# Performance work log

Measured on AMD Instinct MI355X. Metric: run time of the kernel, lower is better.

The kernel has to match this reference:

```python
import jax, jax.numpy as jnp
import numpy as np

HIDDEN = 2048
EMBED = 512
LEN_ACTION = 64   # total size of the NAS search space (embedding rows)
N_VALUES = 16     # number of choices for the queried parameter's head


def gru_cell(x, h, w_ih, w_hh, b_ih, b_hh):
    # PyTorch GRU cell: gates packed as [r, z, n] along dim 0 of weights
    gi = x @ w_ih.T + b_ih          # [1, 3H]
    gh = h @ w_hh.T + b_hh          # [1, 3H]
    i_r, i_z, i_n = jnp.split(gi, 3, axis=-1)
    h_r, h_z, h_n = jnp.split(gh, 3, axis=-1)
    r = jax.nn.sigmoid(i_r + h_r)
    z = jax.nn.sigmoid(i_z + h_z)
    n = jnp.tanh(i_n + r * h_n)
    return (1.0 - z) * n + z * h


def setup_inputs() -> dict:
    key = jax.random.key(0)
    ks = jax.random.split(key, 14)
    s = 0.02
    return {
        "x": jax.random.randint(ks[0], (1,), 0, LEN_ACTION),
        "h_in": jax.random.normal(ks[1], (2, 1, HIDDEN), jnp.float32),
        "emb": jax.random.normal(ks[2], (LEN_ACTION, EMBED), jnp.float32) * s,
        "w_ih0": jax.random.normal(ks[3], (3 * HIDDEN, EMBED), jnp.float32) * s,
        "w_hh0": jax.random.normal(ks[4], (3 * HIDDEN, HIDDEN), jnp.float32) * s,
        "b_ih0": jax.random.normal(ks[5], (3 * HIDDEN,), jnp.float32) * s,
        "b_hh0": jax.random.normal(ks[6], (3 * HIDDEN,), jnp.float32) * s,
        "w_ih1": jax.random.normal(ks[7], (3 * HIDDEN, HIDDEN), jnp.float32) * s,
        "w_hh1": jax.random.normal(ks[8], (3 * HIDDEN, HIDDEN), jnp.float32) * s,
        "b_ih1": jax.random.normal(ks[9], (3 * HIDDEN,), jnp.float32) * s,
        "b_hh1": jax.random.normal(ks[10], (3 * HIDDEN,), jnp.float32) * s,
        "w_head": jax.random.normal(ks[11], (N_VALUES, HIDDEN), jnp.float32) * s,
        "b_head": jax.random.normal(ks[12], (N_VALUES,), jnp.float32) * s,
    }


def reference(x, h_in, emb, w_ih0, w_hh0, b_ih0, b_hh0,
              w_ih1, w_hh1, b_ih1, b_hh1, w_head, b_head):
    e = emb[x]                                    # [1, E] (seq len 1)
    h0 = gru_cell(e, h_in[0], w_ih0, w_hh0, b_ih0, b_hh0)   # [1, H]
    h1 = gru_cell(h0, h_in[1], w_ih1, w_hh1, b_ih1, b_hh1)  # [1, H]
    logits = h1 @ w_head.T + b_head               # [1, N_VALUES]
    probs = jax.nn.softmax(logits, axis=-1)       # Categorical probs
    h_out = jnp.stack([h0, h1], axis=0)           # [num_layers, 1, H]
    return probs, h_out
```

## Files before the change

kernel.cpp:

```cpp
#include <hip/hip_runtime.h>
#include <math.h>

#define HID 2048
#define EMB 512
#define NV 16

__device__ __forceinline__ float wred(float v) {
#pragma unroll
    for (int o = 32; o >= 1; o >>= 1) v += __shfl_down(v, o, 64);
    return v;
}

__device__ __forceinline__ float dot4(float4 a, float4 b) {
    return a.x * b.x + a.y * b.y + a.z * b.z + a.w * b.w;
}

__device__ __forceinline__ float sig(float x) { return 1.0f / (1.0f + __expf(-x)); }

__global__ __launch_bounds__(256) void k1(
    const int* __restrict__ xidx,
    const float* __restrict__ h_in,
    const float* __restrict__ emb,
    const float* __restrict__ w_ih0,
    const float* __restrict__ w_hh0,
    const float* __restrict__ b_ih0,
    const float* __restrict__ b_hh0,
    const float* __restrict__ w_hh1,
    const float* __restrict__ b_hh1,
    float* __restrict__ out,
    float* __restrict__ gh1)
{
    const int tid  = threadIdx.x;
    const int lane = tid & 63;
    const int wv   = tid >> 6;
    const int bid  = blockIdx.x;
    __shared__ float red[4][6];

    float s0 = 0.f, s1 = 0.f, s2 = 0.f, s3 = 0.f, s4 = 0.f, s5 = 0.f;

    if (bid < HID) {
        const int j = bid;
        const float bi_r = b_ih0[j];
        const float bi_z = b_ih0[j + HID];
        const float bi_n = b_ih0[j + 2 * HID];
        const float bh_r = b_hh0[j];
        const float bh_z = b_hh0[j + HID];
        const float bh_n = b_hh0[j + 2 * HID];
        const float hprev = h_in[j];

        const float4* hv  = (const float4*)h_in;
        const float4* wh0 = (const float4*)(w_hh0 + (size_t)j * HID);
        const float4* wh1 = (const float4*)(w_hh0 + (size_t)(j + HID) * HID);
        const float4* wh2 = (const float4*)(w_hh0 + (size_t)(j + 2 * HID) * HID);

        float4 x0 = hv[tid];
        float4 x1 = hv[tid + 256];
        float4 a0 = wh0[tid];
        float4 a1 = wh0[tid + 256];
        float4 b0 = wh1[tid];
        float4 b1 = wh1[tid + 256];
        float4 d0 = wh2[tid];
        float4 d1 = wh2[tid + 256];

        if (tid < 128) {
            const float4* ev  = (const float4*)(emb + (size_t)xidx[0] * EMB);
            const float4* wi0 = (const float4*)(w_ih0 + (size_t)j * EMB);
            const float4* wi1 = (const float4*)(w_ih0 + (size_t)(j + HID) * EMB);
            const float4* wi2 = (const float4*)(w_ih0 + (size_t)(j + 2 * HID) * EMB);
            float4 e4 = ev[tid];
            float4 ia = wi0[tid];
            float4 ib = wi1[tid];
            float4 ic = wi2[tid];
            s0 = dot4(ia, e4);
            s1 = dot4(ib, e4);
            s2 = dot4(ic, e4);
        }

        s3 = dot4(a0, x0) + dot4(a1, x1);
        s4 = dot4(b0, x0) + dot4(b1, x1);
        s5 = dot4(d0, x0) + dot4(d1, x1);

        s0 = wred(s0); s1 = wred(s1); s2 = wred(s2);
        s3 = wred(s3); s4 = wred(s4); s5 = wred(s5);
        if (lane == 0) {
            red[wv][0] = s0; red[wv][1] = s1; red[wv][2] = s2;
            red[wv][3] = s3; red[wv][4] = s4; red[wv][5] = s5;
        }
        __syncthreads();
        if (tid == 0) {
            float ir  = red[0][0] + red[1][0] + red[2][0] + red[3][0] + bi_r;
            float iz  = red[0][1] + red[1][1] + red[2][1] + red[3][1] + bi_z;
            float inn = red[0][2] + red[1][2] + red[2][2] + red[3][2] + bi_n;
            float hr  = red[0][3] + red[1][3] + red[2][3] + red[3][3] + bh_r;
            float hz  = red[0][4] + red[1][4] + red[2][4] + red[3][4] + bh_z;
            float hn  = red[0][5] + red[1][5] + red[2][5] + red[3][5] + bh_n;
            float r = sig(ir + hr);
            float z = sig(iz + hz);
            float n = tanhf(inn + r * hn);
            out[NV + j] = (1.0f - z) * n + z * hprev;
        }
    } else {
        const int j = bid - HID;
        const float bh_r = b_hh1[j];
        const float bh_z = b_hh1[j + HID];
        const float bh_n = b_hh1[j + 2 * HID];

        const float4* hv  = (const float4*)(h_in + HID);
        const float4* wh0 = (const float4*)(w_hh1 + (size_t)j * HID);
        const float4* wh1 = (const float4*)(w_hh1 + (size_t)(j + HID) * HID);
        const float4* wh2 = (const float4*)(w_hh1 + (size_t)(j + 2 * HID) * HID);

        float4 x0 = hv[tid];
        float4 x1 = hv[tid + 256];
        float4 a0 = wh0[tid];
        float4 a1 = wh0[tid + 256];
        float4 b0 = wh1[tid];
        float4 b1 = wh1[tid + 256];
        float4 d0 = wh2[tid];
        float4 d1 = wh2[tid + 256];

        s0 = dot4(a0, x0) + dot4(a1, x1);
        s1 = dot4(b0, x0) + dot4(b1, x1);
        s2 = dot4(d0, x0) + dot4(d1, x1);

        s0 = wred(s0); s1 = wred(s1); s2 = wred(s2);
        if (lane == 0) {
            red[wv][0] = s0; red[wv][1] = s1; red[wv][2] = s2;
        }
        __syncthreads();
        if (tid == 0) {
            gh1[j]           = red[0][0] + red[1][0] + red[2][0] + red[3][0] + bh_r;
            gh1[j + HID]     = red[0][1] + red[1][1] + red[2][1] + red[3][1] + bh_z;
            gh1[j + 2 * HID] = red[0][2] + red[1][2] + red[2][2] + red[3][2] + bh_n;
        }
    }
}

__global__ __launch_bounds__(256) void k2(
    const float* __restrict__ h_in,
    const float* __restrict__ w_ih1,
    const float* __restrict__ b_ih1,
    const float* __restrict__ gh1,
    float* __restrict__ out)
{
    const int tid  = threadIdx.x;
    const int lane = tid & 63;
    const int wv   = tid >> 6;
    const int j    = blockIdx.x;
    __shared__ float red[4][3];

    const float bi_r = b_ih1[j];
    const float bi_z = b_ih1[j + HID];
    const float bi_n = b_ih1[j + 2 * HID];
    const float g_r  = gh1[j];
    const float g_z  = gh1[j + HID];
    const float g_n  = gh1[j + 2 * HID];
    const float hprev = h_in[HID + j];

    const float4* hv  = (const float4*)(out + NV);
    const float4* wi0 = (const float4*)(w_ih1 + (size_t)j * HID);
    const float4* wi1 = (const float4*)(w_ih1 + (size_t)(j + HID) * HID);
    const float4* wi2 = (const float4*)(w_ih1 + (size_t)(j + 2 * HID) * HID);

    float4 x0 = hv[tid];
    float4 x1 = hv[tid + 256];
    float4 a0 = wi0[tid];
    float4 a1 = wi0[tid + 256];
    float4 b0 = wi1[tid];
    float4 b1 = wi1[tid + 256];
    float4 d0 = wi2[tid];
    float4 d1 = wi2[tid + 256];

    float s0 = dot4(a0, x0) + dot4(a1, x1);
    float s1 = dot4(b0, x0) + dot4(b1, x1);
    float s2 = dot4(d0, x0) + dot4(d1, x1);

    s0 = wred(s0); s1 = wred(s1); s2 = wred(s2);
    if (lane == 0) { red[wv][0] = s0; red[wv][1] = s1; red[wv][2] = s2; }
    __syncthreads();
    if (tid == 0) {
        float ir  = red[0][0] + red[1][0] + red[2][0] + red[3][0] + bi_r;
        float iz  = red[0][1] + red[1][1] + red[2][1] + red[3][1] + bi_z;
        float inn = red[0][2] + red[1][2] + red[2][2] + red[3][2] + bi_n;
        float r = sig(ir + g_r);
        float z = sig(iz + g_z);
        float n = tanhf(inn + r * g_n);
        out[NV + HID + j] = (1.0f - z) * n + z * hprev;
    }
}

__global__ __launch_bounds__(256) void k3(
    const float* __restrict__ w_head,
    const float* __restrict__ b_head,
    float* __restrict__ out)
{
    const int tid = threadIdx.x;
    const int row = tid >> 4;
    const int sub = tid & 15;
    const float bh = b_head[row];
    const float4* hv = (const float4*)(out + NV + HID);
    const float4* w  = (const float4*)(w_head + (size_t)row * HID);

    float s = 0.f;
#pragma unroll 4
    for (int c = sub; c < HID / 4; c += 16) {
        float4 x = hv[c];
        float4 a = w[c];
        s += dot4(a, x);
    }
#pragma unroll
    for (int o = 8; o >= 1; o >>= 1) s += __shfl_down(s, o, 16);

    __shared__ float logits[NV];
    if (sub == 0) logits[row] = s + bh;
    __syncthreads();
    if (tid == 0) {
        float m = logits[0];
#pragma unroll
        for (int i = 1; i < NV; ++i) m = fmaxf(m, logits[i]);
        float ex[NV]; float den = 0.f;
#pragma unroll
        for (int i = 0; i < NV; ++i) { ex[i] = __expf(logits[i] - m); den += ex[i]; }
        float inv = 1.0f / den;
#pragma unroll
        for (int i = 0; i < NV; ++i) out[i] = ex[i] * inv;
    }
}

extern "C" void kernel_launch(void* const* d_in, const int* in_sizes, int n_in,
                              void* d_out, int out_size, void* d_ws, size_t ws_size,
                              hipStream_t stream) {
    const int*   x      = (const int*)  d_in[0];
    const float* h_in   = (const float*)d_in[1];
    const float* emb    = (const float*)d_in[2];
    const float* w_ih0  = (const float*)d_in[3];
    const float* w_hh0  = (const float*)d_in[4];
    const float* b_ih0  = (const float*)d_in[5];
    const float* b_hh0  = (const float*)d_in[6];
    const float* w_ih1  = (const float*)d_in[7];
    const float* w_hh1  = (const float*)d_in[8];
    const float* b_ih1  = (const float*)d_in[9];
    const float* b_hh1  = (const float*)d_in[10];
    const float* w_head = (const float*)d_in[11];
    const float* b_head = (const float*)d_in[12];
    float* out = (float*)d_out;
    float* gh1 = (float*)d_ws;

    k1<<<2 * HID, 256, 0, stream>>>(x, h_in, emb, w_ih0, w_hh0, b_ih0, b_hh0,
                                    w_hh1, b_hh1, out, gh1);
    k2<<<HID, 256, 0, stream>>>(h_in, w_ih1, b_ih1, gh1, out);
    k3<<<1, 256, 0, stream>>>(w_head, b_head, out);
}
```

Before: 36.76 us.

## Fuse head/softmax into layer-1 kernel via last-block atomic, two rows per block

Removes the third kernel launch by having the last-finishing block of k2 compute the head logits and softmax, using an atomic counter in workspace that k1 resets. It also halves the grid of both kernels so each 128-thread half-block handles one output row, with more loads in flight per thread. It adds an atomic, a threadfence and an extra barrier, and a single tail block does the serial head work.

```diff
diff --git a/kernel.cpp b/kernel.cpp
--- a/kernel.cpp
+++ b/kernel.cpp
@@ -5,14 +5,14 @@
 #define EMB 512
 #define NV 16
 
+__device__ __forceinline__ float dot4(float4 a, float4 b) {
+    return a.x * b.x + a.y * b.y + a.z * b.z + a.w * b.w;
+}
+
 __device__ __forceinline__ float wred(float v) {
 #pragma unroll
     for (int o = 32; o >= 1; o >>= 1) v += __shfl_down(v, o, 64);
     return v;
-}
-
-__device__ __forceinline__ float dot4(float4 a, float4 b) {
-    return a.x * b.x + a.y * b.y + a.z * b.z + a.w * b.w;
 }
 
 __device__ __forceinline__ float sig(float x) { return 1.0f / (1.0f + __expf(-x)); }
@@ -28,18 +28,20 @@
     const float* __restrict__ w_hh1,
     const float* __restrict__ b_hh1,
     float* __restrict__ out,
-    float* __restrict__ gh1)
+    float* __restrict__ ws)
 {
     const int tid  = threadIdx.x;
+    const int t    = tid & 127;
+    const int half = tid >> 7;
+    const int wave = tid >> 6;
     const int lane = tid & 63;
-    const int wv   = tid >> 6;
     const int bid  = blockIdx.x;
-    __shared__ float red[4][6];
-
-    float s0 = 0.f, s1 = 0.f, s2 = 0.f, s3 = 0.f, s4 = 0.f, s5 = 0.f;
-
-    if (bid < HID) {
-        const int j = bid;
+    __shared__ float red[4][4];
+
+    if (bid == 0 && tid == 0) ((int*)ws)[3 * HID] = 0;
+
+    if (bid < 1024) {
+        const int j = 2 * bid + half;
         const float bi_r = b_ih0[j];
         const float bi_z = b_ih0[j + HID];
         const float bi_n = b_ih0[j + 2 * HID];
@@ -48,90 +50,70 @@
         const float bh_n = b_hh0[j + 2 * HID];
         const float hprev = h_in[j];
 
-        const float4* hv  = (const float4*)h_in;
-        const float4* wh0 = (const float4*)(w_hh0 + (size_t)j * HID);
-        const float4* wh1 = (const float4*)(w_hh0 + (size_t)(j + HID) * HID);
-        const float4* wh2 = (const float4*)(w_hh0 + (size_t)(j + 2 * HID) * HID);
-
-        float4 x0 = hv[tid];
-        float4 x1 = hv[tid + 256];
-        float4 a0 = wh0[tid];
-        float4 a1 = wh0[tid + 256];
-        float4 b0 = wh1[tid];
-        float4 b1 = wh1[tid + 256];
-        float4 d0 = wh2[tid];
-        float4 d1 = wh2[tid + 256];
-
-        if (tid < 128) {
-            const float4* ev  = (const float4*)(emb + (size_t)xidx[0] * EMB);
-            const float4* wi0 = (const float4*)(w_ih0 + (size_t)j * EMB);
-            const float4* wi1 = (const float4*)(w_ih0 + (size_t)(j + HID) * EMB);
-            const float4* wi2 = (const float4*)(w_ih0 + (size_t)(j + 2 * HID) * EMB);
-            float4 e4 = ev[tid];
-            float4 ia = wi0[tid];
-            float4 ib = wi1[tid];
-            float4 ic = wi2[tid];
-            s0 = dot4(ia, e4);
-            s1 = dot4(ib, e4);
-            s2 = dot4(ic, e4);
-        }
-
-        s3 = dot4(a0, x0) + dot4(a1, x1);
-        s4 = dot4(b0, x0) + dot4(b1, x1);
-        s5 = dot4(d0, x0) + dot4(d1, x1);
-
-        s0 = wred(s0); s1 = wred(s1); s2 = wred(s2);
-        s3 = wred(s3); s4 = wred(s4); s5 = wred(s5);
+        const float4* hv = (const float4*)h_in;
+        const float4* wr = (const float4*)(w_hh0 + (size_t)j * HID);
+        const float4* wz = (const float4*)(w_hh0 + (size_t)(j + HID) * HID);
+        const float4* wn = (const float4*)(w_hh0 + (size_t)(j + 2 * HID) * HID);
+        const float4* ev = (const float4*)(emb + (size_t)xidx[0] * EMB);
+        const float4* pir = (const float4*)(w_ih0 + (size_t)j * EMB);
+        const float4* piz = (const float4*)(w_ih0 + (size_t)(j + HID) * EMB);
+        const float4* pin = (const float4*)(w_ih0 + (size_t)(j + 2 * HID) * EMB);
+
+        float4 x0 = hv[t], x1 = hv[t + 128], x2 = hv[t + 256], x3 = hv[t + 384];
+        float4 r0 = wr[t], r1 = wr[t + 128], r2 = wr[t + 256], r3 = wr[t + 384];
+        float4 z0 = wz[t], z1 = wz[t + 128], z2 = wz[t + 256], z3 = wz[t + 384];
+        float4 n0 = wn[t], n1 = wn[t + 128], n2 = wn[t + 256], n3 = wn[t + 384];
+        float4 e4 = ev[t];
+        float4 i0 = pir[t], i1 = piz[t], i2 = pin[t];
+
+        float s_r  = dot4(r0, x0) + dot4(r1, x1) + dot4(r2, x2) + dot4(r3, x3) + dot4(i0, e4);
+        float s_z  = dot4(z0, x0) + dot4(z1, x1) + dot4(z2, x2) + dot4(z3, x3) + dot4(i1, e4);
+        float s_hn = dot4(n0, x0) + dot4(n1, x1) + dot4(n2, x2) + dot4(n3, x3);
+        float s_in = dot4(i2, e4);
+
+        s_r = wred(s_r); s_z = wred(s_z); s_hn = wred(s_hn); s_in = wred(s_in);
         if (lane == 0) {
-            red[wv][0] = s0; red[wv][1] = s1; red[wv][2] = s2;
-            red[wv][3] = s3; red[wv][4] = s4; red[wv][5] = s5;
+            red[wave][0] = s_r; red[wave][1] = s_z; red[wave][2] = s_hn; red[wave][3] = s_in;
         }
         __syncthreads();
-        if (tid == 0) {
-            float ir  = red[0][0] + red[1][0] + red[2][0] + red[3][0] + bi_r;
-            float iz  = red[0][1] + red[1][1] + red[2][1] + red[3][1] + bi_z;
-            float inn = red[0][2] + red[1][2] + red[2][2] + red[3][2] + bi_n;
-            float hr  = red[0][3] + red[1][3] + red[2][3] + red[3][3] + bh_r;
-            float hz  = red[0][4] + red[1][4] + red[2][4] + red[3][4] + bh_z;
-            float hn  = red[0][5] + red[1][5] + red[2][5] + red[3][5] + bh_n;
-            float r = sig(ir + hr);
-            float z = sig(iz + hz);
-            float n = tanhf(inn + r * hn);
+        if (t == 0) {
+            const int w0 = 2 * half, w1 = 2 * half + 1;
+            float r  = sig(red[w0][0] + red[w1][0] + bi_r + bh_r);
+            float z  = sig(red[w0][1] + red[w1][1] + bi_z + bh_z);
+            float hn = red[w0][2] + red[w1][2] + bh_n;
+            float n  = tanhf(red[w0][3] + red[w1][3] + bi_n + r * hn);
             out[NV + j] = (1.0f - z) * n + z * hprev;
         }
     } else {
-        const int j = bid - HID;
-        const float bh_r = b_hh1[j];
-        const float bh_z = b_hh1[j + HID];
-        const float bh_n = b_hh1[j + 2 * HID];
-
-        const float4* hv  = (const float4*)(h_in + HID);
-        const float4* wh0 = (const float4*)(w_hh1 + (size_t)j * HID);
-        const float4* wh1 = (const float4*)(w_hh1 + (size_t)(j + HID) * HID);
-        const float4* wh2 = (const float4*)(w_hh1 + (size_t)(j + 2 * HID) * HID);
-
-        float4 x0 = hv[tid];
-        float4 x1 = hv[tid + 256];
-        float4 a0 = wh0[tid];
-        float4 a1 = wh0[tid + 256];
-        float4 b0 = wh1[tid];
-        float4 b1 = wh1[tid + 256];
-        float4 d0 = wh2[tid];
-        float4 d1 = wh2[tid + 256];
-
-        s0 = dot4(a0, x0) + dot4(a1, x1);
-        s1 = dot4(b0, x0) + dot4(b1, x1);
-        s2 = dot4(d0, x0) + dot4(d1, x1);
-
-        s0 = wred(s0); s1 = wred(s1); s2 = wred(s2);
+        const int j = 2 * (bid - 1024) + half;
+        const float b_r = b_hh1[j];
+        const float b_z = b_hh1[j + HID];
+        const float b_n = b_hh1[j + 2 * HID];
+
+        const float4* hv = (const float4*)(h_in + HID);
+        const float4* wr = (const float4*)(w_hh1 + (size_t)j * HID);
+        const float4* wz = (const float4*)(w_hh1 + (size_t)(j + HID) * HID);
+        const float4* wn = (const float4*)(w_hh1 + (size_t)(j + 2 * HID) * HID);
+
+        float4 x0 = hv[t], x1 = hv[t + 128], x2 = hv[t + 256], x3 = hv[t + 384];
+        float4 r0 = wr[t], r1 = wr[t + 128], r2 = wr[t + 256], r3 = wr[t + 384];
+        float4 z0 = wz[t], z1 = wz[t + 128], z2 = wz[t + 256], z3 = wz[t + 384];
+        float4 n0 = wn[t], n1 = wn[t + 128], n2 = wn[t + 256], n3 = wn[t + 384];
+
+        float s_r = dot4(r0, x0) + dot4(r1, x1) + dot4(r2, x2) + dot4(r3, x3);
+        float s_z = dot4(z0, x0) + dot4(z1, x1) + dot4(z2, x2) + dot4(z3, x3);
+        float s_n = dot4(n0, x0) + dot4(n1, x1) + dot4(n2, x2) + dot4(n3, x3);
+
+        s_r = wred(s_r); s_z = wred(s_z); s_n = wred(s_n);
         if (lane == 0) {
-            red[wv][0] = s0; red[wv][1] = s1; red[wv][2] = s2;
+            red[wave][0] = s_r; red[wave][1] = s_z; red[wave][2] = s_n;
         }
         __syncthreads();
-        if (tid == 0) {
-            gh1[j]           = red[0][0] + red[1][0] + red[2][0] + red[3][0] + bh_r;
-            gh1[j + HID]     = red[0][1] + red[1][1] + red[2][1] + red[3][1] + bh_z;
-            gh1[j + 2 * HID] = red[0][2] + red[1][2] + red[2][2] + red[3][2] + bh_n;
+        if (t == 0) {
+            const int w0 = 2 * half, w1 = 2 * half + 1;
+            ws[j]           = red[w0][0] + red[w1][0] + b_r;
+            ws[j + HID]     = red[w0][1] + red[w1][1] + b_z;
+            ws[j + 2 * HID] = red[w0][2] + red[w1][2] + b_n;
         }
     }
 }
@@ -140,78 +122,78 @@
     const float* __restrict__ h_in,
     const float* __restrict__ w_ih1,
     const float* __restrict__ b_ih1,
-    const float* __restrict__ gh1,
-    float* __restrict__ out)
+    const float* __restrict__ w_head,
+    const float* __restrict__ b_head,
+    float* __restrict__ out,
+    float* __restrict__ ws)
 {
     const int tid  = threadIdx.x;
+    const int t    = tid & 127;
+    const int half = tid >> 7;
+    const int wave = tid >> 6;
     const int lane = tid & 63;
-    const int wv   = tid >> 6;
-    const int j    = blockIdx.x;
+    const int bid  = blockIdx.x;
     __shared__ float red[4][3];
-
+    __shared__ int lastFlag;
+    __shared__ float logits[NV];
+
+    const int j = 2 * bid + half;
     const float bi_r = b_ih1[j];
     const float bi_z = b_ih1[j + HID];
     const float bi_n = b_ih1[j + 2 * HID];
-    const float g_r  = gh1[j];
-    const float g_z  = gh1[j + HID];
-    const float g_n  = gh1[j + 2 * HID];
+    const float g_r  = ws[j];
+    const float g_z  = ws[j + HID];
+    const float g_n  = ws[j + 2 * HID];
     const float hprev = h_in[HID + j];
 
-    const float4* hv  = (const float4*)(out + NV);
-    const float4* wi0 = (const float4*)(w_ih1 + (size_t)j * HID);
-    const float4* wi1 = (const float4*)(w_ih1 + (size_t)(j + HID) * HID);
-    const float4* wi2 = (const float4*)(w_ih1 + (size_t)(j + 2 * HID) * HID);
-
-    float4 x0 = hv[tid];
-    float4 x1 = hv[tid + 256];
-    float4 a0 = wi0[tid];
-    float4 a1 = wi0[tid + 256];
-    float4 b0 = wi1[tid];
-    float4 b1 = wi1[tid + 256];
-    float4 d0 = wi2[tid];
-    float4 d1 = wi2[tid + 256];
-
-    float s0 = dot4(a0, x0) + dot4(a1, x1);
-    float s1 = dot4(b0, x0) + dot4(b1, x1);
-    float s2 = dot4(d0, x0) + dot4(d1, x1);
-
-    s0 = wred(s0); s1 = wred(s1); s2 = wred(s2);
-    if (lane == 0) { red[wv][0] = s0; red[wv][1] = s1; red[wv][2] = s2; }
-    __syncthreads();
+    const float4* hv = (const float4*)(out + NV);
+    const float4* wr = (const float4*)(w_ih1 + (size_t)j * HID);
+    const float4* wz = (const float4*)(w_ih1 + (size_t)(j + HID) * HID);
+    const float4* wn = (const float4*)(w_ih1 + (size_t)(j + 2 * HID) * HID);
+
+    float4 x0 = hv[t], x1 = hv[t + 128], x2 = hv[t + 256], x3 = hv[t + 384];
+    float4 r0 = wr[t], r1 = wr[t + 128], r2 = wr[t + 256], r3 = wr[t + 384];
+    float4 z0 = wz[t], z1 = wz[t + 128], z2 = wz[t + 256], z3 = wz[t + 384];
+    float4 n0 = wn[t], n1 = wn[t + 128], n2 = wn[t + 256], n3 = wn[t + 384];
+
+    float s_r = dot4(r0, x0) + dot4(r1, x1) + dot4(r2, x2) + dot4(r3, x3);
+    float s_z = dot4(z0, x0) + dot4(z1, x1) + dot4(z2, x2) + dot4(z3, x3);
+    float s_n = dot4(n0, x0) + dot4(n1, x1) + dot4(n2, x2) + dot4(n3, x3);
+
+    s_r = wred(s_r); s_z = wred(s_z); s_n = wred(s_n);
+    if (lane == 0) { red[wave][0] = s_r; red[wave][1] = s_z; red[wave][2] = s_n; }
+    __syncthreads();
+    if (t == 0) {
+        const int w0 = 2 * half, w1 = 2 * half + 1;
+        float r = sig(red[w0][0] + red[w1][0] + bi_r + g_r);
+        float z = sig(red[w0][1] + red[w1][1] + bi_z + g_z);
+        float n = tanhf(red[w0][2] + red[w1][2] + bi_n + r * g_n);
+        out[NV + HID + j] = (1.0f - z) * n + z * hprev;
+    }
+    __syncthreads();
+
     if (tid == 0) {
-        float ir  = red[0][0] + red[1][0] + red[2][0] + red[3][0] + bi_r;
-        float iz  = red[0][1] + red[1][1] + red[2][1] + red[3][1] + bi_z;
-        float inn = red[0][2] + red[1][2] + red[2][2] + red[3][2] + bi_n;
-        float r = sig(ir + g_r);
-        float z = sig(iz + g_z);
-        float n = tanhf(inn + r * g_n);
-        out[NV + HID + j] = (1.0f - z) * n + z * hprev;
-    }
-}
-
-__global__ __launch_bounds__(256) void k3(
-    const float* __restrict__ w_head,
-    const float* __restrict__ b_head,
-    float* __restrict__ out)
-{
-    const int tid = threadIdx.x;
+        __threadfence();
+        int* cnt = (int*)ws + 3 * HID;
+        int old = atomicAdd(cnt, 1);
+        lastFlag = (old == (int)gridDim.x - 1);
+    }
+    __syncthreads();
+    if (!lastFlag) return;
+
+    __threadfence();
     const int row = tid >> 4;
     const int sub = tid & 15;
     const float bh = b_head[row];
-    const float4* hv = (const float4*)(out + NV + HID);
-    const float4* w  = (const float4*)(w_head + (size_t)row * HID);
+    const float4* h1v = (const float4*)(out + NV + HID);
+    const float4* w   = (const float4*)(w_head + (size_t)row * HID);
 
     float s = 0.f;
-#pragma unroll 4
-    for (int c = sub; c < HID / 4; c += 16) {
-        float4 x = hv[c];
-        float4 a = w[c];
-        s += dot4(a, x);
-    }
+#pragma unroll 8
+    for (int c = sub; c < HID / 4; c += 16) s += dot4(w[c], h1v[c]);
 #pragma unroll
     for (int o = 8; o >= 1; o >>= 1) s += __shfl_down(s, o, 16);
 
-    __shared__ float logits[NV];
     if (sub == 0) logits[row] = s + bh;
     __syncthreads();
     if (tid == 0) {
@@ -244,10 +226,9 @@
     const float* w_head = (const float*)d_in[11];
     const float* b_head = (const float*)d_in[12];
     float* out = (float*)d_out;
-    float* gh1 = (float*)d_ws;
-
-    k1<<<2 * HID, 256, 0, stream>>>(x, h_in, emb, w_ih0, w_hh0, b_ih0, b_hh0,
-                                    w_hh1, b_hh1, out, gh1);
-    k2<<<HID, 256, 0, stream>>>(h_in, w_ih1, b_ih1, gh1, out);
-    k3<<<1, 256, 0, stream>>>(w_head, b_head, out);
-}
+    float* ws  = (float*)d_ws;
+
+    k1<<<2048, 256, 0, stream>>>(x, h_in, emb, w_ih0, w_hh0, b_ih0, b_hh0,
+                                 w_hh1, b_hh1, out, ws);
+    k2<<<1024, 256, 0, stream>>>(h_in, w_ih1, b_ih1, w_head, b_head, out, ws);
+}
```

After: 65.97 us. 79.5% more time.
